# Kernel optimization log

Hardware: AMD Instinct MI355X
Metric: run time of the kernel (lower is better)

The kernel has to match this reference:

```python
import jax, jax.numpy as jnp
import numpy as np

N = 20000      # nodes
E = 640000     # edges
R = 90         # relations
IN_F = 128     # raw feature dim
HID = 64       # hidden_channels
OUT = 32       # out_channels of conv2
NCLASS = 4
NB = 35        # num_bases (conv1)
EPS = 1e-16    # PyG softmax epsilon


def setup_inputs() -> dict:
    key = jax.random.key(0)
    ks = jax.random.split(key, 16)
    s = 0.1
    return {
        "x": jax.random.normal(ks[0], (N, IN_F), jnp.float32),
        "edge_index": jax.random.randint(ks[1], (2, E), 0, N, jnp.int32),
        "edge_type": jax.random.randint(ks[2], (E,), 0, R, jnp.int32),
        "edge_attr": jax.random.normal(ks[3], (E, 16), jnp.float32),
        # lin1: in_channels -> hidden (no bias)
        "lin1_w": jax.random.normal(ks[4], (IN_F, HID), jnp.float32) * s,
        # conv1: basis decomposition, heads=2, out=20, dim=2 -> H*O=40, H*dim=4
        "att1": jax.random.normal(ks[5], (R, NB), jnp.float32) * s,
        "basis1": jax.random.normal(ks[6], (NB, HID, 40), jnp.float32) * s,
        "q1": jax.random.normal(ks[7], (40, 4), jnp.float32) * s,
        "k1": jax.random.normal(ks[8], (40, 4), jnp.float32) * s,
        "wmod1": jnp.ones((20,), jnp.float32),            # mod='additive' weight (init ones)
        "bias1": jnp.zeros((80,), jnp.float32),            # concat bias: H*dim*O = 80
        # conv2: block-diagonal, in=80, blocks=2, H*O=64, H*dim=2
        "w2": jax.random.normal(ks[9], (R, 2, 40, 32), jnp.float32) * s,
        "q2": jax.random.normal(ks[10], (64, 2), jnp.float32) * s,
        "k2": jax.random.normal(ks[11], (64, 2), jnp.float32) * s,
        "lin_edge_w": jax.random.normal(ks[12], (16, 64), jnp.float32) * s,
        "e2": jax.random.normal(ks[13], (64, 2), jnp.float32) * s,
        # lin2: 2*out -> nclass
        "lin2_w": jax.random.normal(ks[14], (2 * OUT, NCLASS), jnp.float32) * s,
        "lin2_b": jnp.zeros((NCLASS,), jnp.float32),
    }


def segment_softmax(alpha, seg, num_segments):
    # PyG softmax: exp(x - detach(segment_max)) / (segment_sum + 1e-16)
    m = jax.ops.segment_max(alpha, seg, num_segments=num_segments)
    e = jnp.exp(alpha - jax.lax.stop_gradient(m)[seg])
    ssum = jax.ops.segment_sum(e, seg, num_segments=num_segments)
    return e / (ssum[seg] + EPS)


def rgat_forward(x, edge_index, edge_type, edge_attr, lin1_w, att1, basis1,
                 q1, k1, wmod1, bias1, w2, q2, k2, lin_edge_w, e2, lin2_w, lin2_b):
    src, dst = edge_index[0], edge_index[1]   # x_j = x[src], x_i = x[dst]
    n = x.shape[0]
    e = src.shape[0]

    h = x @ lin1_w                            # [N, HID]

    # ---- conv1: basis decomposition, within-relation, multiplicative attn, mod='additive'
    w = jnp.einsum('rb,bio->rio', att1, basis1)          # [R, HID, 40]
    xw = jnp.einsum('ni,rio->rno', h, w)                 # [R, N, 40] (all-relation transform)
    outj = xw[edge_type, src]                            # [E, 40]
    outi = xw[edge_type, dst]                            # [E, 40]
    qi = outi @ q1                                       # [E, 4]
    kj = outj @ k1                                       # [E, 4]
    alpha = qi * kj                                      # multiplicative-self-attention
    seg = dst.astype(jnp.int32) * R + edge_type          # within-relation softmax groups
    alpha = segment_softmax(alpha, seg, n * R)           # [E, 4]
    outj4 = outj.reshape(e, 2, 1, 20)                    # [E, H, 1, O]
    hmod = wmod1 * jnp.broadcast_to(outj4, (e, 2, 2, 20))  # mod='additive' term
    msg = outj4 * alpha.reshape(e, 2, 2, 1) + hmod       # [E, H, dim, O]
    agg = jax.ops.segment_sum(msg, dst, num_segments=n)  # [N, 2, 2, 20]
    h1 = agg.reshape(n, 80) + bias1
    h1 = jax.nn.relu(h1)

    # ---- conv2: block-diagonal, across-relation, additive attn, edge features, no bias
    xb = h1.reshape(n, 2, 40)
    xw2 = jnp.einsum('nbc,rbcd->rnbd', xb, w2).reshape(R, n, 64)  # [R, N, 64]
    outj = xw2[edge_type, src]                           # [E, 64]
    outi = xw2[edge_type, dst]
    qi = outi @ q2                                       # [E, 2]
    kj = outj @ k2
    ae = (edge_attr @ lin_edge_w) @ e2                   # [E, 2]
    alpha = jax.nn.leaky_relu(qi + kj + ae, 0.2)         # additive-self-attention
    alpha = segment_softmax(alpha, dst, n)               # across-relation
    msg = alpha.reshape(e, 2, 1) * outj.reshape(e, 2, 32)
    h2 = jax.ops.segment_sum(msg, dst, num_segments=n).reshape(n, 64)

    out = h2 @ lin2_w + lin2_b
    return jax.nn.log_softmax(out, axis=-1)


def reference(x, edge_index, edge_type, edge_attr, lin1_w, att1, basis1, q1, k1,
              wmod1, bias1, w2, q2, k2, lin_edge_w, e2, lin2_w, lin2_b):
    return rgat_forward(x, edge_index, edge_type, edge_attr, lin1_w, att1, basis1,
                        q1, k1, wmod1, bias1, w2, q2, k2, lin_edge_w, e2, lin2_w, lin2_b)
```

## Files before the change

kernel.cpp:

```cpp
#include <hip/hip_runtime.h>
#include <math.h>

constexpr int NN   = 20000;
constexpr int EE   = 640000;
constexpr int RR   = 90;
constexpr int INF_ = 128;
constexpr int HID  = 64;
constexpr float EPS = 1e-16f;
constexpr int E2   = 646144;

typedef unsigned short u16;
typedef _Float16 f16;
typedef __attribute__((ext_vector_type(8))) short bf16x8;
typedef __attribute__((ext_vector_type(8))) _Float16 f16x8;
typedef __attribute__((ext_vector_type(4))) float f32x4;

__device__ inline u16 f2bf(float f) {
    unsigned int u = __float_as_uint(f);
    unsigned int r = (u + 0x7FFFu + ((u >> 16) & 1u)) >> 16;
    return (u16)r;
}

__device__ inline unsigned f2ord(float f) {
    unsigned u = __float_as_uint(f);
    return (u & 0x80000000u) ? ~u : (u | 0x80000000u);
}
__device__ inline float ord2f(unsigned x) {
    unsigned u = (x & 0x80000000u) ? (x & 0x7FFFFFFFu) : ~x;
    return __uint_as_float(u);
}
#define ORD_NEGINF 0x007FFFFFu

__global__ void k_fillrec(int4* p, int n) {
    int i = blockIdx.x * blockDim.x + threadIdx.x;
    if (i < n) { int4 r; r.x = 0; r.y = 0; r.z = 0; r.w = -1; p[i] = r; }
}

__global__ void k_hist(const int* et, int* hist) {
    __shared__ int lh[RR];
    if (threadIdx.x < RR) lh[threadIdx.x] = 0;
    __syncthreads();
    int i = blockIdx.x * blockDim.x + threadIdx.x;
    if (i < EE) atomicAdd(&lh[et[i]], 1);
    __syncthreads();
    if (threadIdx.x < RR) atomicAdd(&hist[threadIdx.x], lh[threadIdx.x]);
}

__global__ void k_scanPad(const int* hist, int* cursor) {
    if (threadIdx.x == 0) {
        int acc = 0;
        for (int r = 0; r < RR; ++r) {
            cursor[r] = acc;
            acc += (hist[r] + 63) & ~63;
        }
    }
}

__global__ void k_scatter(const int* src, const int* dst, const int* et,
                          int* cursor, int4* sortedR, int* posS) {
    __shared__ int lh[RR];
    __shared__ int lbase[RR];
    if (threadIdx.x < RR) lh[threadIdx.x] = 0;
    __syncthreads();
    int i = blockIdx.x * blockDim.x + threadIdx.x;
    int r = et[i];
    int rank = atomicAdd(&lh[r], 1);
    __syncthreads();
    if (threadIdx.x < RR) {
        int c = lh[threadIdx.x];
        lbase[threadIdx.x] = c ? atomicAdd(&cursor[threadIdx.x], c) : 0;
    }
    __syncthreads();
    int pos = lbase[r] + rank;
    int4 rec; rec.x = src[i]; rec.y = dst[i]; rec.z = r; rec.w = i;
    sortedR[pos] = rec;
    posS[i] = pos;
}

__global__ void k_histD(const int* dst, int* histD) {
    int i = blockIdx.x * blockDim.x + threadIdx.x;
    if (i < EE) atomicAdd(&histD[dst[i]], 1);
}

__global__ void k_scanD(const int* histD, int* rowptrD, int* cursorD) {
    __shared__ int part[256];
    const int CH = (NN + 255) / 256;
    int tid = threadIdx.x;
    int base = tid * CH;
    int s = 0;
    for (int j = 0; j < CH; ++j) {
        int idx = base + j;
        if (idx < NN) s += histD[idx];
    }
    part[tid] = s;
    __syncthreads();
    if (tid == 0) {
        int acc = 0;
        for (int t = 0; t < 256; ++t) { int v = part[t]; part[t] = acc; acc += v; }
    }
    __syncthreads();
    int acc = part[tid];
    for (int j = 0; j < CH; ++j) {
        int idx = base + j;
        if (idx < NN) {
            rowptrD[idx] = acc;
            cursorD[idx] = acc;
            acc += histD[idx];
        }
    }
    if (tid == 0) rowptrD[NN] = EE;
}

__global__ void k_scatterD(const int4* sortedR, int* cursorD, int4* sortedD,
                           int* posD) {
    int i = blockIdx.x * blockDim.x + threadIdx.x;
    if (i >= E2) return;
    int4 rec = sortedR[i];
    if (rec.w < 0) return;
    int pos = atomicAdd(&cursorD[rec.y], 1);
    int4 out; out.x = i; out.y = rec.y; out.z = rec.z; out.w = 0;
    sortedD[pos] = out;
    posD[i] = pos;
}

__global__ void k_w1(const float* att1, const float* basis1, float* w1) {
    int idx = blockIdx.x * blockDim.x + threadIdx.x;
    if (idx >= RR * 2560) return;
    int r = idx / 2560, co = idx - r * 2560;
    float acc = 0.f;
    for (int b = 0; b < 35; ++b) acc += att1[r * 35 + b] * basis1[b * 2560 + co];
    w1[idx] = acc;
}

__global__ void k_wqk1(const float* w1, const float* q1, const float* k1,
                       float* wq1, float* wk1) {
    int idx = blockIdx.x * blockDim.x + threadIdx.x;
    if (idx >= RR * 64 * 4) return;
    int t = idx & 3, c = (idx >> 2) & 63, r = idx >> 8;
    const float* wrow = w1 + (size_t)r * 2560 + c * 40;
    float aq = 0.f, ak = 0.f;
    for (int o = 0; o < 40; ++o) {
        float w = wrow[o];
        aq += w * q1[o * 4 + t];
        ak += w * k1[o * 4 + t];
    }
    wq1[idx] = aq; wk1[idx] = ak;
}

__global__ void k_wqk2(const float* w2, const float* q2, const float* k2,
                       float* wq2, float* wk2) {
    int idx = blockIdx.x * blockDim.x + threadIdx.x;
    if (idx >= RR * 80 * 2) return;
    int t = idx & 1, bc = (idx >> 1) % 80, r = idx / 160;
    int b = bc / 40, c = bc % 40;
    const float* wbase = w2 + (size_t)((r * 2 + b) * 40 + c) * 32;
    float aq = 0.f, ak = 0.f;
    for (int d = 0; d < 32; ++d) {
        float w = wbase[d];
        aq += w * q2[(b * 32 + d) * 2 + t];
        ak += w * k2[(b * 32 + d) * 2 + t];
    }
    wq2[idx] = aq; wk2[idx] = ak;
}

__global__ void k_we(const float* lew, const float* e2, float* we) {
    int idx = threadIdx.x;
    if (idx >= 32) return;
    int i = idx >> 1, t = idx & 1;
    float acc = 0.f;
    for (int j = 0; j < 64; ++j) acc += lew[i * 64 + j] * e2[j * 2 + t];
    we[idx] = acc;
}

__global__ __launch_bounds__(256) void k_ae(const float* ea, const float* weg,
                                            const int* posS, float* aeS) {
    __shared__ float wes[32];
    if (threadIdx.x < 32) wes[threadIdx.x] = weg[threadIdx.x];
    __syncthreads();
    int e = blockIdx.x * 256 + threadIdx.x;
    if (e >= EE) return;
    const float4* ep = (const float4*)(ea + (size_t)e * 16);
    float a0 = 0.f, a1 = 0.f;
#pragma unroll
    for (int cc = 0; cc < 4; ++cc) {
        float4 v = ep[cc];
        const float* vv = (const float*)&v;
#pragma unroll
        for (int j = 0; j < 4; ++j) {
            int ii = cc * 4 + j;
            a0 = fmaf(vv[j], wes[ii * 2 + 0], a0);
            a1 = fmaf(vv[j], wes[ii * 2 + 1], a1);
        }
    }
    float2 av; av.x = a0; av.y = a1;
    *(float2*)(aeS + (size_t)posS[e] * 2) = av;
}

__global__ void k_w1bT(const float* w1, u16* w1bT) {
    int idx = blockIdx.x * blockDim.x + threadIdx.x;
    if (idx >= RR * 48 * 64) return;
    int k = idx & 63, o = (idx >> 6) % 48, r = idx / (48 * 64);
    float v = (o < 40) ? w1[(size_t)r * 2560 + k * 40 + o] : 0.f;
    w1bT[idx] = f2bf(v);
}

__global__ void k_w2bT(const float* w2, u16* w2bT) {
    int idx = blockIdx.x * blockDim.x + threadIdx.x;
    if (idx >= RR * 2 * 32 * 64) return;
    int c = idx & 63, d = (idx >> 6) & 31, b = (idx >> 11) & 1, r = idx >> 12;
    float v = (c < 40) ? w2[((((size_t)r * 2 + b) * 40) + c) * 32 + d] : 0.f;
    w2bT[idx] = f2bf(v);
}

__global__ void k_h(const float* x, const float* lin1_w, f16* hh, u16* hb) {
    __shared__ float xs[INF_];
    int n = blockIdx.x, t = threadIdx.x;
    xs[t]      = x[(size_t)n * INF_ + t];
    xs[t + 64] = x[(size_t)n * INF_ + t + 64];
    __syncthreads();
    float acc = 0.f;
    for (int i = 0; i < INF_; ++i) acc += xs[i] * lin1_w[i * HID + t];
    hh[(size_t)n * HID + t] = (f16)acc;
    hb[(size_t)n * HID + t] = f2bf(acc);
}

__device__ __forceinline__ void attn1_compute(const f16x8* hd, const f16x8* hs,
                                              const float* __restrict__ q,
                                              const float* __restrict__ k,
                                              float* qi, float* kj) {
#pragma unroll
    for (int t = 0; t < 4; ++t) { qi[t] = 0.f; kj[t] = 0.f; }
#pragma unroll
    for (int cc = 0; cc < 8; ++cc) {
        f16x8 a = hd[cc], b = hs[cc];
#pragma unroll
        for (int j = 0; j < 8; ++j) {
            float av = (float)a[j];
            float bv = (float)b[j];
            const float* q4 = q + (cc * 8 + j) * 4;
            const float* k4 = k + (cc * 8 + j) * 4;
#pragma unroll
            for (int t = 0; t < 4; ++t) {
                qi[t] = fmaf(av, q4[t], qi[t]);
                kj[t] = fmaf(bv, k4[t], kj[t]);
            }
        }
    }
}

__global__ __launch_bounds__(256) void k_e1s(const int4* sortedR, const f16* hh,
                                             const float* wq1g, const float* wk1g,
                                             const int* posD, float* alpha1s) {
    __shared__ float qs[256], ks[256];
    int i = blockIdx.x * 256 + threadIdx.x;
    int4 ed = sortedR[i];
    int s = ed.x, d = ed.y, r = ed.z;
    int rFirst = sortedR[(size_t)blockIdx.x * 256].z;
    int rLast  = sortedR[(size_t)blockIdx.x * 256 + 255].z;
    bool allsame = (rFirst == rLast);
    if (allsame) {
        qs[threadIdx.x] = wq1g[(size_t)rFirst * 256 + threadIdx.x];
        ks[threadIdx.x] = wk1g[(size_t)rFirst * 256 + threadIdx.x];
    }
    __syncthreads();
    if (ed.w < 0) return;
    const f16x8* hd = (const f16x8*)(hh + (size_t)d * 64);
    const f16x8* hs = (const f16x8*)(hh + (size_t)s * 64);
    float qi[4], kj[4];
    if (allsame) attn1_compute(hd, hs, qs, ks, qi, kj);
    else         attn1_compute(hd, hs, wq1g + (size_t)r * 256, wk1g + (size_t)r * 256, qi, kj);
    float4 av;
    av.x = qi[0] * kj[0];
    av.y = qi[1] * kj[1];
    av.z = qi[2] * kj[2];
    av.w = qi[3] * kj[3];
    *(float4*)(alpha1s + (size_t)posD[i] * 4) = av;
}

__global__ __launch_bounds__(256) void k_mfma1(const int4* sortedR, const u16* hb,
                                               const u16* w1bT, float* outj1) {
    int wid = threadIdx.x >> 6, l = threadIdx.x & 63;
    int base = blockIdx.x * 64;
    int r = sortedR[base].z;
    int e0 = base + wid * 16;
    int row16 = l & 15, g = l >> 4;
    bf16x8 a[3][2];
#pragma unroll
    for (int mt = 0; mt < 3; ++mt)
#pragma unroll
        for (int ks = 0; ks < 2; ++ks)
            a[mt][ks] = *(const bf16x8*)(w1bT + ((size_t)r * 48 + mt * 16 + row16) * 64 + ks * 32 + g * 8);
    int s = sortedR[e0 + row16].x;
    bf16x8 b0 = *(const bf16x8*)(hb + (size_t)s * 64 + g * 8);
    bf16x8 b1 = *(const bf16x8*)(hb + (size_t)s * 64 + 32 + g * 8);
    f32x4 acc[3];
#pragma unroll
    for (int mt = 0; mt < 3; ++mt) acc[mt] = (f32x4){0.f, 0.f, 0.f, 0.f};
#pragma unroll
    for (int mt = 0; mt < 3; ++mt) {
        acc[mt] = __builtin_amdgcn_mfma_f32_16x16x32_bf16(a[mt][0], b0, acc[mt], 0, 0, 0);
        acc[mt] = __builtin_amdgcn_mfma_f32_16x16x32_bf16(a[mt][1], b1, acc[mt], 0, 0, 0);
    }
    float* orow = outj1 + (size_t)(e0 + row16) * 40;
#pragma unroll
    for (int mt = 0; mt < 3; ++mt) {
        int col = mt * 16 + g * 4;
        if (col < 40) {
            float4 v; v.x = acc[mt][0]; v.y = acc[mt][1]; v.z = acc[mt][2]; v.w = acc[mt][3];
            *(float4*)(orow + col) = v;
        }
    }
}

__global__ __launch_bounds__(256) void k_aggr1(const int4* sortedD, const int* rowptrD,
                                               const float* outj1, const float* alpha1s,
                                               const float* wmod, const float* bias1,
                                               f16* h1h, u16* h1b) {
    __shared__ unsigned smax[4][RR * 4];
    __shared__ float    ssum[4][RR * 4];
    int wid = threadIdx.x >> 6;
    int lane = threadIdx.x & 63;
    int w = blockIdx.x * 4 + wid;
    int beg = rowptrD[w], end = rowptrD[w + 1];
    unsigned* mx = smax[wid];
    float*    sm = ssum[wid];
    for (int j = beg + lane; j < end; j += 64) {
        int rb = sortedD[j].z * 4;
        mx[rb + 0] = ORD_NEGINF; mx[rb + 1] = ORD_NEGINF;
        mx[rb + 2] = ORD_NEGINF; mx[rb + 3] = ORD_NEGINF;
        sm[rb + 0] = 0.f; sm[rb + 1] = 0.f; sm[rb + 2] = 0.f; sm[rb + 3] = 0.f;
    }
    __syncthreads();
    for (int j = beg + lane; j < end; j += 64) {
        float4 a = *(const float4*)(alpha1s + (size_t)j * 4);
        int rb = sortedD[j].z * 4;
        atomicMax(&mx[rb + 0], f2ord(a.x));
        atomicMax(&mx[rb + 1], f2ord(a.y));
        atomicMax(&mx[rb + 2], f2ord(a.z));
        atomicMax(&mx[rb + 3], f2ord(a.w));
    }
    __syncthreads();
    for (int j = beg + lane; j < end; j += 64) {
        float4 a = *(const float4*)(alpha1s + (size_t)j * 4);
        int rb = sortedD[j].z * 4;
        atomicAdd(&sm[rb + 0], __expf(a.x - ord2f(mx[rb + 0])));
        atomicAdd(&sm[rb + 1], __expf(a.y - ord2f(mx[rb + 1])));
        atomicAdd(&sm[rb + 2], __expf(a.z - ord2f(mx[rb + 2])));
        atomicAdd(&sm[rb + 3], __expf(a.w - ord2f(mx[rb + 3])));
    }
    __syncthreads();
    for (int t = lane; t < RR * 4; t += 64) sm[t] = 1.f / (sm[t] + EPS);
    __syncthreads();
    int hh = lane >= 20 ? 1 : 0;
    int oo = lane - hh * 20;
    float acc0 = 0.f, acc1 = 0.f, accw = 0.f;
    if (lane < 40) {
        for (int j = beg; j < end; ++j) {
            int4 rec = sortedD[j];
            int i = rec.x, rb = rec.z * 4 + hh * 2;
            float v = outj1[(size_t)i * 40 + lane];
            float2 a = *(const float2*)(alpha1s + (size_t)j * 4 + hh * 2);
            float e0 = __expf(a.x - ord2f(mx[rb]));
            float e1 = __expf(a.y - ord2f(mx[rb + 1]));
            acc0 = fmaf(v, e0 * sm[rb], acc0);
            acc1 = fmaf(v, e1 * sm[rb + 1], acc1);
            accw += v;
        }
        float wm = wmod[oo];
        int b0 = hh * 40 + oo;
        float o0 = fmaxf(acc0 + wm * accw + bias1[b0], 0.f);
        float o1 = fmaxf(acc1 + wm * accw + bias1[b0 + 20], 0.f);
        h1h[(size_t)w * 80 + b0]      = (f16)o0;
        h1h[(size_t)w * 80 + b0 + 20] = (f16)o1;
        h1b[((size_t)w * 2 + hh) * 64 + oo]      = f2bf(o0);
        h1b[((size_t)w * 2 + hh) * 64 + oo + 20] = f2bf(o1);
    } else {
        int lam = lane - 40;
        h1b[((size_t)w * 2 + 0) * 64 + 40 + lam] = 0;
        h1b[((size_t)w * 2 + 1) * 64 + 40 + lam] = 0;
    }
}

__device__ __forceinline__ void attn2_compute(const f16x8* hd, const f16x8* hs,
                                              const float* __restrict__ q,
                                              const float* __restrict__ k,
                                              float* a) {
    a[0] = 0.f; a[1] = 0.f;
#pragma unroll
    for (int cc = 0; cc < 10; ++cc) {
        f16x8 xv = hd[cc], yv = hs[cc];
#pragma unroll
        for (int j = 0; j < 8; ++j) {
            float x = (float)xv[j];
            float y = (float)yv[j];
            int bc = cc * 8 + j;
            a[0] = fmaf(x, q[bc * 2 + 0], fmaf(y, k[bc * 2 + 0], a[0]));
            a[1] = fmaf(x, q[bc * 2 + 1], fmaf(y, k[bc * 2 + 1], a[1]));
        }
    }
}

__global__ __launch_bounds__(256) void k_f1s(const int4* sortedR, const f16* h1h,
                                             const float* wq2g, const float* wk2g,
                                             const float* aeS, const int* posD,
                                             float* alpha2s) {
    __shared__ float qs[160], ks[160];
    int i = blockIdx.x * 256 + threadIdx.x;
    int4 ed = sortedR[i];
    int s = ed.x, d = ed.y, r = ed.z, e = ed.w;
    int rFirst = sortedR[(size_t)blockIdx.x * 256].z;
    int rLast  = sortedR[(size_t)blockIdx.x * 256 + 255].z;
    bool allsame = (rFirst == rLast);
    if (allsame && threadIdx.x < 160) {
        qs[threadIdx.x] = wq2g[(size_t)rFirst * 160 + threadIdx.x];
        ks[threadIdx.x] = wk2g[(size_t)rFirst * 160 + threadIdx.x];
    }
    __syncthreads();
    if (e < 0) return;
    const f16x8* hd = (const f16x8*)(h1h + (size_t)d * 80);
    const f16x8* hs = (const f16x8*)(h1h + (size_t)s * 80);
    float a[2];
    if (allsame) attn2_compute(hd, hs, qs, ks, a);
    else         attn2_compute(hd, hs, wq2g + (size_t)r * 160, wk2g + (size_t)r * 160, a);
    float2 aev = *(const float2*)(aeS + (size_t)i * 2);
    a[0] += aev.x;
    a[1] += aev.y;
    a[0] = a[0] > 0.f ? a[0] : 0.2f * a[0];
    a[1] = a[1] > 0.f ? a[1] : 0.2f * a[1];
    float2 av; av.x = a[0]; av.y = a[1];
    *(float2*)(alpha2s + (size_t)posD[i] * 2) = av;
}

__global__ __launch_bounds__(256) void k_mfma2(const int4* sortedR, const u16* h1b,
                                               const u16* w2bT, float* outj2) {
    int wid = threadIdx.x >> 6, l = threadIdx.x & 63;
    int base = blockIdx.x * 64;
    int r = sortedR[base].z;
    int e0 = base + wid * 16;
    int row16 = l & 15, g = l >> 4;
    bf16x8 a[2][2][2];
#pragma unroll
    for (int b = 0; b < 2; ++b)
#pragma unroll
        for (int mt = 0; mt < 2; ++mt)
#pragma unroll
            for (int ks = 0; ks < 2; ++ks)
                a[b][mt][ks] = *(const bf16x8*)(w2bT + ((((size_t)r * 2 + b) * 32) + mt * 16 + row16) * 64 + ks * 32 + g * 8);
    int s = sortedR[e0 + row16].x;
    bf16x8 bb[2][2];
#pragma unroll
    for (int b = 0; b < 2; ++b)
#pragma unroll
        for (int ks = 0; ks < 2; ++ks)
            bb[b][ks] = *(const bf16x8*)(h1b + ((size_t)s * 2 + b) * 64 + ks * 32 + g * 8);
    f32x4 acc[2][2];
#pragma unroll
    for (int b = 0; b < 2; ++b)
#pragma unroll
        for (int mt = 0; mt < 2; ++mt) acc[b][mt] = (f32x4){0.f, 0.f, 0.f, 0.f};
#pragma unroll
    for (int b = 0; b < 2; ++b)
#pragma unroll
        for (int mt = 0; mt < 2; ++mt) {
            acc[b][mt] = __builtin_amdgcn_mfma_f32_16x16x32_bf16(a[b][mt][0], bb[b][0], acc[b][mt], 0, 0, 0);
            acc[b][mt] = __builtin_amdgcn_mfma_f32_16x16x32_bf16(a[b][mt][1], bb[b][1], acc[b][mt], 0, 0, 0);
        }
    float* orow = outj2 + (size_t)(e0 + row16) * 64;
#pragma unroll
    for (int b = 0; b < 2; ++b)
#pragma unroll
        for (int mt = 0; mt < 2; ++mt) {
            float4 v; v.x = acc[b][mt][0]; v.y = acc[b][mt][1]; v.z = acc[b][mt][2]; v.w = acc[b][mt][3];
            *(float4*)(orow + b * 32 + mt * 16 + g * 4) = v;
        }
}

__global__ __launch_bounds__(256) void k_aggr2(const int4* sortedD, const int* rowptrD,
                                               const float* outj2, const float* alpha2s,
                                               float* h2) {
    int w = blockIdx.x * 4 + (threadIdx.x >> 6);
    int lane = threadIdx.x & 63;
    if (w >= NN) return;
    int beg = rowptrD[w], end = rowptrD[w + 1];
    float m0 = -INFINITY, m1 = -INFINITY;
    for (int j = beg + lane; j < end; j += 64) {
        float2 a = *(const float2*)(alpha2s + (size_t)j * 2);
        m0 = fmaxf(m0, a.x); m1 = fmaxf(m1, a.y);
    }
#pragma unroll
    for (int off = 32; off; off >>= 1) {
        m0 = fmaxf(m0, __shfl_xor(m0, off));
        m1 = fmaxf(m1, __shfl_xor(m1, off));
    }
    float s0 = 0.f, s1 = 0.f;
    for (int j = beg + lane; j < end; j += 64) {
        float2 a = *(const float2*)(alpha2s + (size_t)j * 2);
        s0 += __expf(a.x - m0); s1 += __expf(a.y - m1);
    }
#pragma unroll
    for (int off = 32; off; off >>= 1) {
        s0 += __shfl_xor(s0, off);
        s1 += __shfl_xor(s1, off);
    }
    int b = lane >> 5;
    float mb = b ? m1 : m0;
    float rs = 1.f / ((b ? s1 : s0) + EPS);
    float acc = 0.f;
    for (int j = beg; j < end; ++j) {
        int i = sortedD[j].x;
        float v = outj2[(size_t)i * 64 + lane];
        float a = alpha2s[(size_t)j * 2 + b];
        acc = fmaf(v, __expf(a - mb) * rs, acc);
    }
    h2[(size_t)w * 64 + lane] = acc;
}

__global__ void k_out(const float* h2, const float* lin2_w, const float* lin2_b,
                      float* out) {
    int n = blockIdx.x * blockDim.x + threadIdx.x;
    if (n >= NN) return;
    float o[4] = {lin2_b[0], lin2_b[1], lin2_b[2], lin2_b[3]};
    const float* hr = h2 + (size_t)n * 64;
    for (int c = 0; c < 64; ++c) {
        float hv = hr[c];
#pragma unroll
        for (int t = 0; t < 4; ++t) o[t] = fmaf(hv, lin2_w[c * 4 + t], o[t]);
    }
    float m = fmaxf(fmaxf(o[0], o[1]), fmaxf(o[2], o[3]));
    float s = __expf(o[0] - m) + __expf(o[1] - m) + __expf(o[2] - m) + __expf(o[3] - m);
    float lse = m + logf(s);
#pragma unroll
    for (int t = 0; t < 4; ++t) out[(size_t)n * 4 + t] = o[t] - lse;
}

extern "C" void kernel_launch(void* const* d_in, const int* in_sizes, int n_in,
                              void* d_out, int out_size, void* d_ws, size_t ws_size,
                              hipStream_t stream) {
    const float* x        = (const float*)d_in[0];
    const int*   eidx     = (const int*)d_in[1];
    const int*   etype    = (const int*)d_in[2];
    const float* eattr    = (const float*)d_in[3];
    const float* lin1_w   = (const float*)d_in[4];
    const float* att1     = (const float*)d_in[5];
    const float* basis1   = (const float*)d_in[6];
    const float* q1       = (const float*)d_in[7];
    const float* k1       = (const float*)d_in[8];
    const float* wmod1    = (const float*)d_in[9];
    const float* bias1    = (const float*)d_in[10];
    const float* w2       = (const float*)d_in[11];
    const float* q2       = (const float*)d_in[12];
    const float* k2       = (const float*)d_in[13];
    const float* lew      = (const float*)d_in[14];
    const float* e2i      = (const float*)d_in[15];
    const float* lin2_w   = (const float*)d_in[16];
    const float* lin2_b   = (const float*)d_in[17];

    const int* src = eidx;
    const int* dst = eidx + EE;

    float* W = (float*)d_ws;
    float* w1      = W;   W += 230400;
    float* wq1     = W;   W += 23040;
    float* wk1     = W;   W += 23040;
    float* wq2     = W;   W += 14400;
    float* wk2     = W;   W += 14400;
    float* we      = W;   W += 32;
    float* h2      = W;   W += (size_t)NN * 64;
    float* aeS     = W;   W += (size_t)E2 * 2;
    f16*   hh      = (f16*)W;   W += (size_t)NN * 64 / 2;
    f16*   h1h     = (f16*)W;   W += (size_t)NN * 80 / 2;
    u16*   hb      = (u16*)W;   W += (size_t)NN * 64 / 2;
    u16*   h1b     = (u16*)W;   W += (size_t)NN * 128 / 2;
    u16*   w1bT    = (u16*)W;   W += (size_t)RR * 48 * 64 / 2;
    u16*   w2bT    = (u16*)W;   W += (size_t)RR * 2 * 32 * 64 / 2;
    float* uni     = W;   W += (size_t)E2 * 64;
    float* outj1   = uni;
    float* alpha1s = uni + (size_t)E2 * 40;
    float* outj2   = uni;
    float* alpha2s = W;   W += (size_t)EE * 2;
    int4*  sortedR = (int4*)W;
    int*   I = (int*)W;   I += (size_t)E2 * 4;
    int4*  sortedD = (int4*)I;  I += (size_t)E2 * 4;
    int*   posS    = I;   I += EE;
    int*   posD    = I;   I += E2;
    int*   rowptrD = I;   I += NN + 1;
    int*   cursorD = I;   I += NN;
    int*   histD   = I;   I += NN;
    int*   hist    = I;   I += 128;
    int*   cursor  = I;   I += 128;

    hipMemsetAsync(histD, 0, (size_t)(NN + 256) * 4, stream);
    k_fillrec<<<E2 / 256, 256, 0, stream>>>(sortedR, E2);

    k_hist<<<EE / 256, 256, 0, stream>>>(etype, hist);
    k_scanPad<<<1, 64, 0, stream>>>(hist, cursor);
    k_scatter<<<EE / 256, 256, 0, stream>>>(src, dst, etype, cursor, sortedR, posS);
    k_histD<<<EE / 256, 256, 0, stream>>>(dst, histD);
    k_scanD<<<1, 256, 0, stream>>>(histD, rowptrD, cursorD);
    k_scatterD<<<E2 / 256, 256, 0, stream>>>(sortedR, cursorD, sortedD, posD);

    k_w1<<<(RR * 2560 + 255) / 256, 256, 0, stream>>>(att1, basis1, w1);
    k_wqk1<<<(RR * 256 + 255) / 256, 256, 0, stream>>>(w1, q1, k1, wq1, wk1);
    k_wqk2<<<(RR * 160 + 255) / 256, 256, 0, stream>>>(w2, q2, k2, wq2, wk2);
    k_we<<<1, 32, 0, stream>>>(lew, e2i, we);
    k_ae<<<EE / 256, 256, 0, stream>>>(eattr, we, posS, aeS);
    k_w1bT<<<(RR * 48 * 64) / 256, 256, 0, stream>>>(w1, w1bT);
    k_w2bT<<<(RR * 2 * 32 * 64) / 256, 256, 0, stream>>>(w2, w2bT);
    k_h<<<NN, 64, 0, stream>>>(x, lin1_w, hh, hb);

    k_e1s<<<E2 / 256, 256, 0, stream>>>(sortedR, hh, wq1, wk1, posD, alpha1s);
    k_mfma1<<<E2 / 64, 256, 0, stream>>>(sortedR, hb, w1bT, outj1);
    k_aggr1<<<NN / 4, 256, 0, stream>>>(sortedD, rowptrD, outj1, alpha1s,
                                        wmod1, bias1, h1h, h1b);

    k_f1s<<<E2 / 256, 256, 0, stream>>>(sortedR, h1h, wq2, wk2, aeS, posD, alpha2s);
    k_mfma2<<<E2 / 64, 256, 0, stream>>>(sortedR, h1b, w2bT, outj2);
    k_aggr2<<<(NN + 3) / 4, 256, 0, stream>>>(sortedD, rowptrD, outj2, alpha2s, h2);

    k_out<<<(NN + 255) / 256, 256, 0, stream>>>(h2, lin2_w, lin2_b, (float*)d_out);
}
```

Baseline: 699.3 us.

## Store per-edge messages in fp16 at dst-sorted positions and drop sortedD

The MFMA kernels now scatter their per-edge outputs, converted to fp16, directly to destination-sorted positions through posD. The aggregation kernels then read them contiguously instead of gathering through an int4 sortedD index. sortedD is replaced by a 16-bit relation array, and the shared-memory softmax tables use a stride of 5, likely to reduce LDS bank conflicts. This cuts the bytes of the large intermediate buffers and turns random gathers into streaming reads. The costs are scattered writes in the MFMA kernels and fp16 precision on the messages.

```diff
diff --git a/kernel.cpp b/kernel.cpp
--- a/kernel.cpp
+++ b/kernel.cpp
@@ -13,6 +13,7 @@
 typedef _Float16 f16;
 typedef __attribute__((ext_vector_type(8))) short bf16x8;
 typedef __attribute__((ext_vector_type(8))) _Float16 f16x8;
+typedef __attribute__((ext_vector_type(4))) _Float16 f16x4;
 typedef __attribute__((ext_vector_type(4))) float f32x4;
 
 __device__ inline u16 f2bf(float f) {
@@ -111,16 +112,15 @@
     if (tid == 0) rowptrD[NN] = EE;
 }
 
-__global__ void k_scatterD(const int4* sortedR, int* cursorD, int4* sortedD,
-                           int* posD) {
+__global__ void k_scatterD(const int4* sortedR, int* cursorD, int* posD,
+                           u16* relD) {
     int i = blockIdx.x * blockDim.x + threadIdx.x;
     if (i >= E2) return;
     int4 rec = sortedR[i];
     if (rec.w < 0) return;
     int pos = atomicAdd(&cursorD[rec.y], 1);
-    int4 out; out.x = i; out.y = rec.y; out.z = rec.z; out.w = 0;
-    sortedD[pos] = out;
     posD[i] = pos;
+    relD[pos] = (u16)rec.z;
 }
 
 __global__ void k_w1(const float* att1, const float* basis1, float* w1) {
@@ -277,8 +277,9 @@
     *(float4*)(alpha1s + (size_t)posD[i] * 4) = av;
 }
 
-__global__ __launch_bounds__(256) void k_mfma1(const int4* sortedR, const u16* hb,
-                                               const u16* w1bT, float* outj1) {
+__global__ __launch_bounds__(256) void k_mfma1(const int4* sortedR, const int* posD,
+                                               const u16* hb, const u16* w1bT,
+                                               f16* outj1h) {
     int wid = threadIdx.x >> 6, l = threadIdx.x & 63;
     int base = blockIdx.x * 64;
     int r = sortedR[base].z;
@@ -290,7 +291,8 @@
 #pragma unroll
         for (int ks = 0; ks < 2; ++ks)
             a[mt][ks] = *(const bf16x8*)(w1bT + ((size_t)r * 48 + mt * 16 + row16) * 64 + ks * 32 + g * 8);
-    int s = sortedR[e0 + row16].x;
+    int4 er = sortedR[e0 + row16];
+    int s = er.x;
     bf16x8 b0 = *(const bf16x8*)(hb + (size_t)s * 64 + g * 8);
     bf16x8 b1 = *(const bf16x8*)(hb + (size_t)s * 64 + 32 + g * 8);
     f32x4 acc[3];
@@ -301,23 +303,27 @@
         acc[mt] = __builtin_amdgcn_mfma_f32_16x16x32_bf16(a[mt][0], b0, acc[mt], 0, 0, 0);
         acc[mt] = __builtin_amdgcn_mfma_f32_16x16x32_bf16(a[mt][1], b1, acc[mt], 0, 0, 0);
     }
-    float* orow = outj1 + (size_t)(e0 + row16) * 40;
+    if (er.w < 0) return;
+    int pd = posD[e0 + row16];
+    f16* orow = outj1h + (size_t)pd * 40;
 #pragma unroll
     for (int mt = 0; mt < 3; ++mt) {
         int col = mt * 16 + g * 4;
         if (col < 40) {
-            float4 v; v.x = acc[mt][0]; v.y = acc[mt][1]; v.z = acc[mt][2]; v.w = acc[mt][3];
-            *(float4*)(orow + col) = v;
-        }
-    }
-}
-
-__global__ __launch_bounds__(256) void k_aggr1(const int4* sortedD, const int* rowptrD,
-                                               const float* outj1, const float* alpha1s,
+            f16x4 v;
+            v[0] = (f16)acc[mt][0]; v[1] = (f16)acc[mt][1];
+            v[2] = (f16)acc[mt][2]; v[3] = (f16)acc[mt][3];
+            *(f16x4*)(orow + col) = v;
+        }
+    }
+}
+
+__global__ __launch_bounds__(256) void k_aggr1(const u16* relD, const int* rowptrD,
+                                               const f16* outj1h, const float* alpha1s,
                                                const float* wmod, const float* bias1,
                                                f16* h1h, u16* h1b) {
-    __shared__ unsigned smax[4][RR * 4];
-    __shared__ float    ssum[4][RR * 4];
+    __shared__ unsigned smax[4][RR * 5];
+    __shared__ float    ssum[4][RR * 5];
     int wid = threadIdx.x >> 6;
     int lane = threadIdx.x & 63;
     int w = blockIdx.x * 4 + wid;
@@ -325,7 +331,7 @@
     unsigned* mx = smax[wid];
     float*    sm = ssum[wid];
     for (int j = beg + lane; j < end; j += 64) {
-        int rb = sortedD[j].z * 4;
+        int rb = relD[j] * 5;
         mx[rb + 0] = ORD_NEGINF; mx[rb + 1] = ORD_NEGINF;
         mx[rb + 2] = ORD_NEGINF; mx[rb + 3] = ORD_NEGINF;
         sm[rb + 0] = 0.f; sm[rb + 1] = 0.f; sm[rb + 2] = 0.f; sm[rb + 3] = 0.f;
@@ -333,7 +339,7 @@
     __syncthreads();
     for (int j = beg + lane; j < end; j += 64) {
         float4 a = *(const float4*)(alpha1s + (size_t)j * 4);
-        int rb = sortedD[j].z * 4;
+        int rb = relD[j] * 5;
         atomicMax(&mx[rb + 0], f2ord(a.x));
         atomicMax(&mx[rb + 1], f2ord(a.y));
         atomicMax(&mx[rb + 2], f2ord(a.z));
@@ -342,24 +348,23 @@
     __syncthreads();
     for (int j = beg + lane; j < end; j += 64) {
         float4 a = *(const float4*)(alpha1s + (size_t)j * 4);
-        int rb = sortedD[j].z * 4;
+        int rb = relD[j] * 5;
         atomicAdd(&sm[rb + 0], __expf(a.x - ord2f(mx[rb + 0])));
         atomicAdd(&sm[rb + 1], __expf(a.y - ord2f(mx[rb + 1])));
         atomicAdd(&sm[rb + 2], __expf(a.z - ord2f(mx[rb + 2])));
         atomicAdd(&sm[rb + 3], __expf(a.w - ord2f(mx[rb + 3])));
     }
     __syncthreads();
-    for (int t = lane; t < RR * 4; t += 64) sm[t] = 1.f / (sm[t] + EPS);
-    __syncthreads();
-    int hh = lane >= 20 ? 1 : 0;
-    int oo = lane - hh * 20;
+    for (int t = lane; t < RR * 5; t += 64) sm[t] = 1.f / (sm[t] + EPS);
+    __syncthreads();
+    int hh2 = lane >= 20 ? 1 : 0;
+    int oo = lane - hh2 * 20;
     float acc0 = 0.f, acc1 = 0.f, accw = 0.f;
     if (lane < 40) {
         for (int j = beg; j < end; ++j) {
-            int4 rec = sortedD[j];
-            int i = rec.x, rb = rec.z * 4 + hh * 2;
-            float v = outj1[(size_t)i * 40 + lane];
-            float2 a = *(const float2*)(alpha1s + (size_t)j * 4 + hh * 2);
+            int rb = relD[j] * 5 + hh2 * 2;
+            float v = (float)outj1h[(size_t)j * 40 + lane];
+            float2 a = *(const float2*)(alpha1s + (size_t)j * 4 + hh2 * 2);
             float e0 = __expf(a.x - ord2f(mx[rb]));
             float e1 = __expf(a.y - ord2f(mx[rb + 1]));
             acc0 = fmaf(v, e0 * sm[rb], acc0);
@@ -367,13 +372,13 @@
             accw += v;
         }
         float wm = wmod[oo];
-        int b0 = hh * 40 + oo;
+        int b0 = hh2 * 40 + oo;
         float o0 = fmaxf(acc0 + wm * accw + bias1[b0], 0.f);
         float o1 = fmaxf(acc1 + wm * accw + bias1[b0 + 20], 0.f);
         h1h[(size_t)w * 80 + b0]      = (f16)o0;
         h1h[(size_t)w * 80 + b0 + 20] = (f16)o1;
-        h1b[((size_t)w * 2 + hh) * 64 + oo]      = f2bf(o0);
-        h1b[((size_t)w * 2 + hh) * 64 + oo + 20] = f2bf(o1);
+        h1b[((size_t)w * 2 + hh2) * 64 + oo]      = f2bf(o0);
+        h1b[((size_t)w * 2 + hh2) * 64 + oo + 20] = f2bf(o1);
     } else {
         int lam = lane - 40;
         h1b[((size_t)w * 2 + 0) * 64 + 40 + lam] = 0;
@@ -431,8 +436,9 @@
     *(float2*)(alpha2s + (size_t)posD[i] * 2) = av;
 }
 
-__global__ __launch_bounds__(256) void k_mfma2(const int4* sortedR, const u16* h1b,
-                                               const u16* w2bT, float* outj2) {
+__global__ __launch_bounds__(256) void k_mfma2(const int4* sortedR, const int* posD,
+                                               const u16* h1b, const u16* w2bT,
+                                               f16* outj2h) {
     int wid = threadIdx.x >> 6, l = threadIdx.x & 63;
     int base = blockIdx.x * 64;
     int r = sortedR[base].z;
@@ -446,7 +452,8 @@
 #pragma unroll
             for (int ks = 0; ks < 2; ++ks)
                 a[b][mt][ks] = *(const bf16x8*)(w2bT + ((((size_t)r * 2 + b) * 32) + mt * 16 + row16) * 64 + ks * 32 + g * 8);
-    int s = sortedR[e0 + row16].x;
+    int4 er = sortedR[e0 + row16];
+    int s = er.x;
     bf16x8 bb[2][2];
 #pragma unroll
     for (int b = 0; b < 2; ++b)
@@ -465,19 +472,22 @@
             acc[b][mt] = __builtin_amdgcn_mfma_f32_16x16x32_bf16(a[b][mt][0], bb[b][0], acc[b][mt], 0, 0, 0);
             acc[b][mt] = __builtin_amdgcn_mfma_f32_16x16x32_bf16(a[b][mt][1], bb[b][1], acc[b][mt], 0, 0, 0);
         }
-    float* orow = outj2 + (size_t)(e0 + row16) * 64;
+    if (er.w < 0) return;
+    int pd = posD[e0 + row16];
+    f16* orow = outj2h + (size_t)pd * 64;
 #pragma unroll
     for (int b = 0; b < 2; ++b)
 #pragma unroll
         for (int mt = 0; mt < 2; ++mt) {
-            float4 v; v.x = acc[b][mt][0]; v.y = acc[b][mt][1]; v.z = acc[b][mt][2]; v.w = acc[b][mt][3];
-            *(float4*)(orow + b * 32 + mt * 16 + g * 4) = v;
-        }
-}
-
-__global__ __launch_bounds__(256) void k_aggr2(const int4* sortedD, const int* rowptrD,
-                                               const float* outj2, const float* alpha2s,
-                                               float* h2) {
+            f16x4 v;
+            v[0] = (f16)acc[b][mt][0]; v[1] = (f16)acc[b][mt][1];
+            v[2] = (f16)acc[b][mt][2]; v[3] = (f16)acc[b][mt][3];
+            *(f16x4*)(orow + b * 32 + mt * 16 + g * 4) = v;
+        }
+}
+
+__global__ __launch_bounds__(256) void k_aggr2(const int* rowptrD, const f16* outj2h,
+                                               const float* alpha2s, float* h2) {
     int w = blockIdx.x * 4 + (threadIdx.x >> 6);
     int lane = threadIdx.x & 63;
     if (w >= NN) return;
@@ -507,8 +517,7 @@
     float rs = 1.f / ((b ? s1 : s0) + EPS);
     float acc = 0.f;
     for (int j = beg; j < end; ++j) {
-        int i = sortedD[j].x;
-        float v = outj2[(size_t)i * 64 + lane];
+        float v = (float)outj2h[(size_t)j * 64 + lane];
         float a = alpha2s[(size_t)j * 2 + b];
         acc = fmaf(v, __expf(a - mb) * rs, acc);
     }
@@ -573,14 +582,15 @@
     u16*   h1b     = (u16*)W;   W += (size_t)NN * 128 / 2;
     u16*   w1bT    = (u16*)W;   W += (size_t)RR * 48 * 64 / 2;
     u16*   w2bT    = (u16*)W;   W += (size_t)RR * 2 * 32 * 64 / 2;
-    float* uni     = W;   W += (size_t)E2 * 64;
-    float* outj1   = uni;
-    float* alpha1s = uni + (size_t)E2 * 40;
-    float* outj2   = uni;
+    float* uni     = W;   W += (size_t)EE * 20 + (size_t)EE * 4;
+    f16*   outj1h  = (f16*)uni;
+    float* alpha1s = uni + (size_t)EE * 20;
+    f16*   outj2h  = (f16*)uni;
+    W += (size_t)EE * 8;
     float* alpha2s = W;   W += (size_t)EE * 2;
     int4*  sortedR = (int4*)W;
     int*   I = (int*)W;   I += (size_t)E2 * 4;
-    int4*  sortedD = (int4*)I;  I += (size_t)E2 * 4;
+    u16*   relD    = (u16*)I;   I += (size_t)E2 / 2;
     int*   posS    = I;   I += EE;
     int*   posD    = I;   I += E2;
     int*   rowptrD = I;   I += NN + 1;
@@ -597,7 +607,7 @@
     k_scatter<<<EE / 256, 256, 0, stream>>>(src, dst, etype, cursor, sortedR, posS);
     k_histD<<<EE / 256, 256, 0, stream>>>(dst, histD);
     k_scanD<<<1, 256, 0, stream>>>(histD, rowptrD, cursorD);
-    k_scatterD<<<E2 / 256, 256, 0, stream>>>(sortedR, cursorD, sortedD, posD);
+    k_scatterD<<<E2 / 256, 256, 0, stream>>>(sortedR, cursorD, posD, relD);
 
     k_w1<<<(RR * 2560 + 255) / 256, 256, 0, stream>>>(att1, basis1, w1);
     k_wqk1<<<(RR * 256 + 255) / 256, 256, 0, stream>>>(w1, q1, k1, wq1, wk1);
@@ -609,13 +619,13 @@
     k_h<<<NN, 64, 0, stream>>>(x, lin1_w, hh, hb);
 
     k_e1s<<<E2 / 256, 256, 0, stream>>>(sortedR, hh, wq1, wk1, posD, alpha1s);
-    k_mfma1<<<E2 / 64, 256, 0, stream>>>(sortedR, hb, w1bT, outj1);
-    k_aggr1<<<NN / 4, 256, 0, stream>>>(sortedD, rowptrD, outj1, alpha1s,
+    k_mfma1<<<E2 / 64, 256, 0, stream>>>(sortedR, posD, hb, w1bT, outj1h);
+    k_aggr1<<<NN / 4, 256, 0, stream>>>(relD, rowptrD, outj1h, alpha1s,
                                         wmod1, bias1, h1h, h1b);
 
     k_f1s<<<E2 / 256, 256, 0, stream>>>(sortedR, h1h, wq2, wk2, aeS, posD, alpha2s);
-    k_mfma2<<<E2 / 64, 256, 0, stream>>>(sortedR, h1b, w2bT, outj2);
-    k_aggr2<<<(NN + 3) / 4, 256, 0, stream>>>(sortedD, rowptrD, outj2, alpha2s, h2);
+    k_mfma2<<<E2 / 64, 256, 0, stream>>>(sortedR, posD, h1b, w2bT, outj2h);
+    k_aggr2<<<(NN + 3) / 4, 256, 0, stream>>>(rowptrD, outj2h, alpha2s, h2);
 
     k_out<<<(NN + 255) / 256, 256, 0, stream>>>(h2, lin2_w, lin2_b, (float*)d_out);
 }
```

After: 640.5 us. -8.4%, faster.
